# Performance work log

Hardware: AMD Instinct MI355X
Metric: run time of the kernel (lower is better)

Reference implementation:

```python
import jax, jax.numpy as jnp
import numpy as np

B, H, E, V = 128, 1024, 1024, 40000
L, S, A = 256, 10, 10
L_S, L_A = 1.0, 1.0  # s_copy_lambda / a_copy_lambda
NEG = -1e24


def setup_inputs():
    key = jax.random.key(0)
    ks = jax.random.split(key, 32)
    n = lambda i, shape: jax.random.normal(ks[i], shape, dtype=jnp.float32)
    p = lambda i, shape: jax.random.normal(ks[i], shape, dtype=jnp.float32) * 0.02
    rnn_in = 3 * E + H  # embed + history ctx (H) + state ctx (E) + action ctx (E)
    return {
        "inp": n(0, (B, 1, E)),
        "hidden": n(1, (1, B, H)),
        "hs_vectors": n(2, (B, L, H)),
        "state_gumbel_prob": jax.random.uniform(ks[3], (B, S, V), dtype=jnp.float32),
        "state_gumbel_embed": n(4, (B, S, E)),
        "action_gumbel_prob": jax.random.uniform(ks[5], (B, A, V), dtype=jnp.float32),
        "action_gumbel_embed": n(6, (B, A, E)),
        "history_lens": jax.random.randint(ks[7], (B,), 1, L + 1),
        "history_word_indices": jax.random.randint(ks[8], (B, L), 0, V),
        # history word mlp-attention
        "Wq_hist": p(9, (H, H)), "bq_hist": jnp.zeros((H,), jnp.float32),
        "Wm_hist": p(10, (H, H)), "v_hist": p(11, (H,)),
        # init_s_attn / init_a_attn (query H, memory E)
        "Wq_s": p(12, (H, H)), "bq_s": jnp.zeros((H,), jnp.float32),
        "Wm_s": p(13, (E, H)), "v_s": p(14, (H,)),
        "Wq_a": p(15, (H, H)), "bq_a": jnp.zeros((H,), jnp.float32),
        "Wm_a": p(16, (E, H)), "v_a": p(17, (H,)),
        # sparse_copy_attn (memory E+1)
        "Wq_sc": p(18, (H, H)), "bq_sc": jnp.zeros((H,), jnp.float32),
        "Wm_sc": p(19, (E + 1, H)), "v_sc": p(20, (H,)),
        # GRU (torch layout: [3H, in], gate order r,z,n)
        "W_ih": p(21, (3 * H, rnn_in)), "W_hh": p(22, (3 * H, H)),
        "b_ih": jnp.zeros((3 * H,), jnp.float32), "b_hh": jnp.zeros((3 * H,), jnp.float32),
        # output projection
        "W_out": p(23, (H, V)), "b_out": jnp.zeros((V,), jnp.float32),
    }


def _mlp_scores(q, mem, Wq, bq, Wm, v):
    # q: [B,1,H], mem: [B,L,M] -> additive-attention logits [B,1,L]
    t = jnp.tanh((q @ Wq + bq) + (mem @ Wm))  # [B,L,H]
    return (t @ v)[:, None, :]


def reference(inp, hidden, hs_vectors, state_gumbel_prob, state_gumbel_embed,
              action_gumbel_prob, action_gumbel_embed, history_lens,
              history_word_indices, Wq_hist, bq_hist, Wm_hist, v_hist,
              Wq_s, bq_s, Wm_s, v_s, Wq_a, bq_a, Wm_a, v_a,
              Wq_sc, bq_sc, Wm_sc, v_sc, W_ih, W_hh, b_ih, b_hh, W_out, b_out):
    q0 = jnp.transpose(hidden, (1, 0, 2))  # [B,1,H]
    # --- history word attention (masked mlp attention) ---
    hist_scores = _mlp_scores(q0, hs_vectors, Wq_hist, bq_hist, Wm_hist, v_hist)
    valid = jnp.arange(L)[None, None, :] < history_lens[:, None, None]
    hist_scores = jnp.where(valid, hist_scores, NEG)
    c_his = jax.nn.softmax(hist_scores, axis=-1) @ hs_vectors  # [B,1,H]
    # --- init_consult over state / action gumbel embeddings ---
    sw = jax.nn.softmax(_mlp_scores(q0, state_gumbel_embed, Wq_s, bq_s, Wm_s, v_s), axis=-1)
    c_state = sw @ state_gumbel_embed  # [B,1,E]
    aw = jax.nn.softmax(_mlp_scores(q0, action_gumbel_embed, Wq_a, bq_a, Wm_a, v_a), axis=-1)
    c_action = aw @ action_gumbel_embed  # [B,1,E]
    x = jnp.concatenate([inp, c_his, c_state, c_action], axis=-1)[:, 0, :]  # [B,3E+H]
    # --- single-step GRU cell (torch semantics, gate order r,z,n) ---
    h0 = hidden[0]
    gi = x @ W_ih.T + b_ih
    gh = h0 @ W_hh.T + b_hh
    ir, iz, inn = jnp.split(gi, 3, axis=-1)
    hr, hz, hn = jnp.split(gh, 3, axis=-1)
    r = jax.nn.sigmoid(ir + hr)
    z = jax.nn.sigmoid(iz + hz)
    nact = jnp.tanh(inn + r * hn)
    h_new = (1.0 - z) * nact + z * h0  # [B,H]
    # --- vocab logits + copy logits, joint softmax ---
    gene_logits = h_new @ W_out + b_out  # [B,V]
    cq = h_new[:, None, :]
    hs_logits = jnp.einsum('bqh,blh->bql', cq, hs_vectors)[:, 0, :]  # dot attn, [B,L]
    s_tag = jnp.zeros((B, S, 1), jnp.float32)
    a_tag = jnp.ones((B, A, 1), jnp.float32)
    st_logits = _mlp_scores(cq, jnp.concatenate([state_gumbel_embed, s_tag], -1), Wq_sc, bq_sc, Wm_sc, v_sc)[:, 0, :]
    ac_logits = _mlp_scores(cq, jnp.concatenate([action_gumbel_embed, a_tag], -1), Wq_sc, bq_sc, Wm_sc, v_sc)[:, 0, :]
    all_logits = jnp.concatenate([gene_logits, hs_logits, st_logits, ac_logits], axis=-1)
    wp = jax.nn.softmax(all_logits, axis=-1)  # [B, V+L+S+A]
    gene_p = wp[:, :V]
    hs_w = wp[:, V:V + L]
    st_w = wp[:, V + L:V + L + S]
    ac_w = wp[:, V + L + S:]
    # --- copy-distribution mixing ---
    scp = jnp.einsum('bs,bsv->bv', st_w, state_gumbel_prob)
    acp = jnp.einsum('ba,bav->bv', ac_w, action_gumbel_prob)
    gene_p = gene_p + L_S * scp + L_A * acp
    copy_p = jnp.zeros((B, V), jnp.float32).at[jnp.arange(B)[:, None], history_word_indices].add(hs_w)
    out = jnp.log(gene_p + copy_p)[:, None, :]  # [B,1,V]
    return out, h_new[None]
```

## Files before the change

kernel.cpp:

```cpp
#include <hip/hip_runtime.h>
#include <stdint.h>

typedef __attribute__((ext_vector_type(4))) float f32x4;
typedef __attribute__((ext_vector_type(2))) unsigned int u32x2;
typedef __attribute__((ext_vector_type(4))) unsigned int u32x4;
typedef __attribute__((ext_vector_type(8))) short bf16x8;

#define BV (128*40000)

__device__ __forceinline__ unsigned rne_bf16(float f) {
    unsigned x = __float_as_uint(f);
    return ((x + 0x7FFFu + ((x >> 16) & 1u)) >> 16) & 0xFFFFu;
}
__device__ __forceinline__ unsigned pack2(float a, float b) {
    return rne_bf16(a) | (rne_bf16(b) << 16);
}
__device__ __forceinline__ float bf2f(unsigned u) {
    return __uint_as_float((u & 0xFFFFu) << 16);
}
__device__ __forceinline__ float sigm(float x) { return 1.0f / (1.0f + expf(-x)); }

__device__ __forceinline__ void gload16(const void* g, void* l) {
    __builtin_amdgcn_global_load_lds(
        (const __attribute__((address_space(1))) unsigned*)g,
        (__attribute__((address_space(3))) unsigned*)l, 16, 0, 0);
}

template<int EPI>
__device__ __forceinline__ void mgemm(
    const unsigned short* __restrict__ A, const unsigned short* __restrict__ Bt,
    float* __restrict__ out, const float* __restrict__ rb,
    const float* __restrict__ cb1, const float* __restrict__ cb2,
    const float* __restrict__ vvec,
    int m0, int n0, int kb, int ke, int ldk, int ldc, int rpb)
{
    __shared__ unsigned short As[2][4096];
    __shared__ unsigned short Bs[2][4096];
    const int t = threadIdx.x, lane = t & 63, wv = t >> 6;
    const int l16 = lane & 15, lq = lane >> 4;
    const int wm = wv >> 1, wn = wv & 1;

    const int srow = lane >> 2, scol = (lane & 3) << 3;
    const unsigned short* gA0 = A + (size_t)(m0 + (wv << 4) + srow) * ldk + kb + scol;
    const unsigned short* gA1 = gA0 + (size_t)64 * ldk;
    const unsigned short* gB0 = Bt + (size_t)(n0 + (wv << 4) + srow) * ldk + kb + scol;
    const unsigned short* gB1 = gB0 + (size_t)64 * ldk;
    unsigned short* lA0 = &As[0][wv << 9];
    unsigned short* lA1 = &As[0][(wv + 4) << 9];
    unsigned short* lB0 = &Bs[0][wv << 9];
    unsigned short* lB1 = &Bs[0][(wv + 4) << 9];

    f32x4 acc[4][4];
#pragma unroll
    for (int i = 0; i < 4; ++i)
#pragma unroll
        for (int j = 0; j < 4; ++j) acc[i][j] = (f32x4){0.f, 0.f, 0.f, 0.f};

    const int NS = (ke - kb) >> 5;
    gload16(gA0, lA0); gload16(gA1, lA1);
    gload16(gB0, lB0); gload16(gB1, lB1);

    for (int s = 0; s < NS; ++s) {
        __syncthreads();
        if (s + 1 < NS) {
            const int nb = (s + 1) & 1, ko = (s + 1) << 5;
            gload16(gA0 + ko, lA0 + (nb << 12)); gload16(gA1 + ko, lA1 + (nb << 12));
            gload16(gB0 + ko, lB0 + (nb << 12)); gload16(gB1 + ko, lB1 + (nb << 12));
        }
        const unsigned short* ab = As[s & 1];
        const unsigned short* bb = Bs[s & 1];
        bf16x8 af[4], bfv[4];
#pragma unroll
        for (int i = 0; i < 4; ++i)
            af[i] = *(const bf16x8*)(ab + (((wm << 6) + (i << 4) + l16) << 5) + (lq << 3));
#pragma unroll
        for (int i = 0; i < 4; ++i)
            bfv[i] = *(const bf16x8*)(bb + (((wn << 6) + (i << 4) + l16) << 5) + (lq << 3));
#pragma unroll
        for (int mf = 0; mf < 4; ++mf)
#pragma unroll
            for (int nf = 0; nf < 4; ++nf)
                acc[mf][nf] = __builtin_amdgcn_mfma_f32_16x16x32_bf16(af[mf], bfv[nf], acc[mf][nf], 0, 0, 0);
    }

    if (EPI == 1) {
#pragma unroll
        for (int mf = 0; mf < 4; ++mf) {
#pragma unroll
            for (int r = 0; r < 4; ++r) {
                int gr = m0 + (wm << 6) + (mf << 4) + (lq << 2) + r;
                const float* rbp = rb + (size_t)(gr / rpb) * 1024;
                float s = 0.0f;
#pragma unroll
                for (int nf = 0; nf < 4; ++nf) {
                    int gc = n0 + (wn << 6) + (nf << 4) + l16;
                    float xv = acc[mf][nf][r] + rbp[gc] + cb1[gc];
                    if (cb2) xv += cb2[gc];
                    s += tanhf(xv) * vvec[gc];
                }
#pragma unroll
                for (int msk = 1; msk < 16; msk <<= 1) s += __shfl_xor(s, msk, 64);
                if (l16 == 0) atomicAdd(&out[gr], s);
            }
        }
    } else {
#pragma unroll
        for (int mf = 0; mf < 4; ++mf) {
            int gr0 = m0 + (wm << 6) + (mf << 4) + (lq << 2);
#pragma unroll
            for (int nf = 0; nf < 4; ++nf) {
                int gc = n0 + (wn << 6) + (nf << 4) + l16;
#pragma unroll
                for (int r = 0; r < 4; ++r)
                    atomicAdd(&out[(size_t)(gr0 + r) * ldc + gc], acc[mf][nf][r]);
            }
        }
    }
}

__device__ __forceinline__ void gene_body(
    const unsigned short* __restrict__ hnb, const float* __restrict__ Wout,
    const float* __restrict__ b_out, float* __restrict__ out, int n0)
{
    __shared__ unsigned short As[2][4096];
    __shared__ unsigned short Bs[2][4096];
    const int t = threadIdx.x, lane = t & 63, wv = t >> 6;
    const int l16 = lane & 15, lq = lane >> 4;
    const int wm = wv >> 1, wn = wv & 1;

    const int srow = lane >> 2, scol = (lane & 3) << 3;
    const unsigned short* gA0 = hnb + (size_t)((wv << 4) + srow) * 1024 + scol;
    const unsigned short* gA1 = gA0 + (size_t)64 * 1024;
    unsigned short* lA0 = &As[0][wv << 9];
    unsigned short* lA1 = &As[0][(wv + 4) << 9];

    const int bn = t & 127, kh = t >> 7;
    const bool ok = (n0 + bn) < 40000;
    const float* gB = Wout + (size_t)(kh * 16) * 40000 + (n0 + bn);

    f32x4 acc[4][4];
#pragma unroll
    for (int i = 0; i < 4; ++i)
#pragma unroll
        for (int j = 0; j < 4; ++j) acc[i][j] = (f32x4){0.f, 0.f, 0.f, 0.f};

    auto stageB = [&](int buf, int ko) {
        const float* src = gB + (size_t)ko * 40000;
        float f[16];
#pragma unroll
        for (int j = 0; j < 16; ++j) f[j] = ok ? src[(size_t)j * 40000] : 0.0f;
        u32x4* d = (u32x4*)&Bs[buf][bn * 32 + kh * 16];
        d[0] = (u32x4){pack2(f[0],f[1]), pack2(f[2],f[3]), pack2(f[4],f[5]), pack2(f[6],f[7])};
        d[1] = (u32x4){pack2(f[8],f[9]), pack2(f[10],f[11]), pack2(f[12],f[13]), pack2(f[14],f[15])};
    };

    gload16(gA0, lA0); gload16(gA1, lA1); stageB(0, 0);
    for (int s = 0; s < 32; ++s) {
        __syncthreads();
        if (s + 1 < 32) {
            const int nb = (s + 1) & 1, ko = (s + 1) << 5;
            gload16(gA0 + ko, lA0 + (nb << 12)); gload16(gA1 + ko, lA1 + (nb << 12));
            stageB(nb, ko);
        }
        const unsigned short* ab = As[s & 1];
        const unsigned short* bb = Bs[s & 1];
        bf16x8 af[4], bfv[4];
#pragma unroll
        for (int i = 0; i < 4; ++i)
            af[i] = *(const bf16x8*)(ab + (((wm << 6) + (i << 4) + l16) << 5) + (lq << 3));
#pragma unroll
        for (int i = 0; i < 4; ++i)
            bfv[i] = *(const bf16x8*)(bb + (((wn << 6) + (i << 4) + l16) << 5) + (lq << 3));
#pragma unroll
        for (int mf = 0; mf < 4; ++mf)
#pragma unroll
            for (int nf = 0; nf < 4; ++nf)
                acc[mf][nf] = __builtin_amdgcn_mfma_f32_16x16x32_bf16(af[mf], bfv[nf], acc[mf][nf], 0, 0, 0);
    }
#pragma unroll
    for (int mf = 0; mf < 4; ++mf) {
        int gr0 = (wm << 6) + (mf << 4) + (lq << 2);
#pragma unroll
        for (int nf = 0; nf < 4; ++nf) {
            int gc = n0 + (wn << 6) + (nf << 4) + l16;
            if (gc < 40000) {
                float bo = b_out[gc];
#pragma unroll
                for (int r = 0; r < 4; ++r)
                    out[(size_t)(gr0 + r) * 40000 + gc] = acc[mf][nf][r] + bo;
            }
        }
    }
}

__global__ __launch_bounds__(256) void k_hist_att(
    const unsigned short* hs, const unsigned short* WmhT, const int* lens,
    const float* qh_h, const float* bq_h, const float* v_h, float* hsc,
    const unsigned short* se, const unsigned short* ae,
    const unsigned short* WmsT, const unsigned short* WmaT,
    const float* qh_s, const float* qh_a, const float* bq_s, const float* bq_a,
    const float* v_s, const float* v_a, float* stsc, float* acsc) {
    int id = blockIdx.x;
    if (id < 2048) {
        int p = id & 255, n = id >> 8;
        int b = p >> 1, l0 = (p & 1) << 7;
        if (lens[b] <= l0) return;
        mgemm<1>(hs, WmhT, hsc, qh_h, bq_h, nullptr, v_h, p << 7, n << 7, 0, 1024, 1024, 0, 256);
    } else {
        int r = id - 2048;
        int z = r / 80; r -= z * 80;
        int y = r >> 3, x = r & 7;
        if (z == 0)
            mgemm<1>(se, WmsT, stsc, qh_s, bq_s, nullptr, v_s, y * 128, x * 128, 0, 1024, 1024, 0, 10);
        else
            mgemm<1>(ae, WmaT, acsc, qh_a, bq_a, nullptr, v_a, y * 128, x * 128, 0, 1024, 1024, 0, 10);
    }
}

__global__ __launch_bounds__(256) void k_stac3(
    const unsigned short* se, const unsigned short* ae, const unsigned short* WmscT,
    const float* tagrow, const float* qsc, const float* bq_sc, const float* v_sc,
    float* stlg, float* aclg) {
    if (blockIdx.z == 0)
        mgemm<1>(se, WmscT, stlg, qsc, bq_sc, nullptr, v_sc, blockIdx.y * 128, blockIdx.x * 128, 0, 1024, 1024, 0, 10);
    else
        mgemm<1>(ae, WmscT, aclg, qsc, bq_sc, tagrow, v_sc, blockIdx.y * 128, blockIdx.x * 128, 0, 1024, 1024, 0, 10);
}

__global__ __launch_bounds__(256) void k_qh4(
    const unsigned short* q0, const unsigned short* W0, const unsigned short* W1,
    const unsigned short* W2, float* o0, float* o1, float* o2) {
    const unsigned short* W = W0; float* o = o0;
    if (blockIdx.z == 1) { W = W1; o = o1; }
    if (blockIdx.z == 2) { W = W2; o = o2; }
    int kb = blockIdx.y << 8;
    mgemm<2>(q0, W, o, nullptr, nullptr, nullptr, nullptr, 0, blockIdx.x * 128, kb, kb + 256, 1024, 1024, 1);
}

__global__ __launch_bounds__(256) void k_gigh2(
    const unsigned short* xb, const unsigned short* q0,
    const unsigned short* Wih, const unsigned short* Whh, float* gi, float* gh) {
    if (blockIdx.z == 0) {
        int kb = blockIdx.y << 9;
        mgemm<2>(xb, Wih, gi, nullptr, nullptr, nullptr, nullptr, 0, blockIdx.x * 128, kb, kb + 512, 4096, 3072, 1);
    } else {
        if (blockIdx.y >= 2) return;
        int kb = blockIdx.y << 9;
        mgemm<2>(q0, Whh, gh, nullptr, nullptr, nullptr, nullptr, 0, blockIdx.x * 128, kb, kb + 512, 1024, 3072, 1);
    }
}

__global__ __launch_bounds__(256) void k_qsc_gene(
    const unsigned short* hnb, const unsigned short* WqscT, float* qsc,
    const float* Wout, const float* b_out, float* out) {
    int id = blockIdx.x;
    if (id < 16) {
        int x = id & 7, kb = (id >> 3) << 9;
        mgemm<2>(hnb, WqscT, qsc, nullptr, nullptr, nullptr, nullptr, 0, x * 128, kb, kb + 512, 1024, 1024, 1);
    } else {
        gene_body(hnb, Wout, b_out, out, (id - 16) << 7);
    }
}

struct CvtArgs { const float* s[6]; unsigned short* d[6]; int pre[7]; };
__global__ __launch_bounds__(256) void k_cvt_all(CvtArgs a) {
    int total = a.pre[6];
    for (int i = blockIdx.x * 256 + threadIdx.x; i < total; i += gridDim.x * 256) {
        int seg = 0;
        while (i >= a.pre[seg + 1]) ++seg;
        int loc = i - a.pre[seg];
        const f32x4* s4 = (const f32x4*)a.s[seg] + (size_t)loc * 2;
        f32x4 q0 = s4[0], q1 = s4[1];
        ((u32x4*)a.d[seg])[loc] =
            (u32x4){pack2(q0[0],q0[1]), pack2(q0[2],q0[3]), pack2(q1[0],q1[1]), pack2(q1[2],q1[3])};
    }
}

struct TrArgs { const float* s[8]; unsigned short* d[8]; };
__global__ __launch_bounds__(256) void k_trcvt(TrArgs a) {
    __shared__ float tile[64][65];
    const float* in = a.s[blockIdx.z];
    unsigned short* ot = a.d[blockIdx.z];
    int k0 = blockIdx.y << 6, n0 = blockIdx.x << 6;
    int tr = threadIdx.x >> 6, tc = threadIdx.x & 63;
#pragma unroll
    for (int i = 0; i < 16; ++i) {
        int r = (i << 2) + tr;
        tile[r][tc] = in[(size_t)(k0 + r) * 1024 + n0 + tc];
    }
    __syncthreads();
#pragma unroll
    for (int i = 0; i < 16; ++i) {
        int r = (i << 2) + tr;
        ot[(size_t)(n0 + r) * 1024 + k0 + tc] = (unsigned short)rne_bf16(tile[tc][r]);
    }
}

__device__ __forceinline__ void softmax10(const float* src, float* dst) {
    float m = src[0];
    for (int i = 1; i < 10; ++i) m = fmaxf(m, src[i]);
    float z = 0.f, e[10];
    for (int i = 0; i < 10; ++i) { e[i] = expf(src[i] - m); z += e[i]; }
    float iz = 1.0f / z;
    for (int i = 0; i < 10; ++i) dst[i] = e[i] * iz;
}

__global__ __launch_bounds__(256) void k_ctx(
    const float* __restrict__ scores, const int* __restrict__ lens,
    const unsigned short* __restrict__ hs,
    const float* __restrict__ inp, const float* __restrict__ st_sc, const float* __restrict__ ac_sc,
    const unsigned short* __restrict__ se, const unsigned short* __restrict__ ae,
    unsigned short* __restrict__ xb) {
    int b = blockIdx.x, t = threadIdx.x;
    __shared__ float w[256];
    __shared__ float red[256];
    __shared__ float sw[10], aw[10];
    int len = lens[b];
    float s = scores[b * 256 + t];
    bool valid = t < len;
    red[t] = valid ? s : -3.0e38f;
    __syncthreads();
    for (int st = 128; st > 0; st >>= 1) { if (t < st) red[t] = fmaxf(red[t], red[t + st]); __syncthreads(); }
    float m = red[0];
    __syncthreads();
    float e = valid ? expf(s - m) : 0.0f;
    red[t] = e;
    __syncthreads();
    for (int st = 128; st > 0; st >>= 1) { if (t < st) red[t] += red[t + st]; __syncthreads(); }
    float Z = red[0];
    __syncthreads();
    w[t] = e / Z;
    if (t == 0) softmax10(st_sc + b * 10, sw);
    if (t == 64) softmax10(ac_sc + b * 10, aw);
    f32x4 iv = ((const f32x4*)(inp + (size_t)b * 1024))[t];
    *((u32x2*)(xb + (size_t)b * 4096) + t) = (u32x2){pack2(iv[0], iv[1]), pack2(iv[2], iv[3])};
    __syncthreads();
    float a0 = 0.f, a1 = 0.f, a2 = 0.f, a3 = 0.f;
    for (int l = 0; l < 256; ++l) {
        float wl = w[l];
        if (wl == 0.0f) continue;
        u32x2 u = *((const u32x2*)(hs + ((size_t)b * 256 + l) * 1024) + t);
        a0 += wl * bf2f(u[0]); a1 += wl * bf2f(u[0] >> 16);
        a2 += wl * bf2f(u[1]); a3 += wl * bf2f(u[1] >> 16);
    }
    *((u32x2*)(xb + (size_t)b * 4096 + 1024) + t) = (u32x2){pack2(a0, a1), pack2(a2, a3)};
    float cs0=0,cs1=0,cs2=0,cs3=0, ca0=0,ca1=0,ca2=0,ca3=0;
#pragma unroll
    for (int q = 0; q < 10; ++q) {
        u32x2 us = *((const u32x2*)(se + ((size_t)b * 10 + q) * 1024) + t);
        u32x2 ua = *((const u32x2*)(ae + ((size_t)b * 10 + q) * 1024) + t);
        float ws = sw[q], wa = aw[q];
        cs0 += ws * bf2f(us[0]); cs1 += ws * bf2f(us[0] >> 16);
        cs2 += ws * bf2f(us[1]); cs3 += ws * bf2f(us[1] >> 16);
        ca0 += wa * bf2f(ua[0]); ca1 += wa * bf2f(ua[0] >> 16);
        ca2 += wa * bf2f(ua[1]); ca3 += wa * bf2f(ua[1] >> 16);
    }
    *((u32x2*)(xb + (size_t)b * 4096 + 2048) + t) = (u32x2){pack2(cs0, cs1), pack2(cs2, cs3)};
    *((u32x2*)(xb + (size_t)b * 4096 + 3072) + t) = (u32x2){pack2(ca0, ca1), pack2(ca2, ca3)};
}

__global__ __launch_bounds__(1024) void k_gruhsl(
    const float* __restrict__ gi, const float* __restrict__ gh,
    const float* __restrict__ b_ih, const float* __restrict__ b_hh,
    const float* __restrict__ h0, float* __restrict__ hnew,
    unsigned short* __restrict__ hnb,
    const unsigned short* __restrict__ hs, float* __restrict__ hsl) {
    int b = blockIdx.x, j = threadIdx.x;
    size_t i = (size_t)b * 1024 + j;
    const float* gib = gi + (size_t)b * 3072;
    const float* ghb = gh + (size_t)b * 3072;
    float r = sigm(gib[j] + b_ih[j] + ghb[j] + b_hh[j]);
    float z = sigm(gib[1024 + j] + b_ih[1024 + j] + ghb[1024 + j] + b_hh[1024 + j]);
    float hn = ghb[2048 + j] + b_hh[2048 + j];
    float n = tanhf(gib[2048 + j] + b_ih[2048 + j] + r * hn);
    float h = (1.0f - z) * n + z * h0[i];
    hnew[i] = h;
    hnb[i] = (unsigned short)rne_bf16(h);
    __shared__ float hsm[1024];
    hsm[j] = h;
    __syncthreads();
    int wave = j >> 6, lane = j & 63;
    float hr[16];
#pragma unroll
    for (int k = 0; k < 16; ++k) hr[k] = hsm[lane * 16 + k];
    for (int l = wave; l < 256; l += 16) {
        const u32x4* row = (const u32x4*)(hs + ((size_t)b * 256 + l) * 1024);
        u32x4 u0 = row[lane * 2], u1 = row[lane * 2 + 1];
        float s = hr[0]*bf2f(u0[0]) + hr[1]*bf2f(u0[0]>>16) + hr[2]*bf2f(u0[1]) + hr[3]*bf2f(u0[1]>>16)
                + hr[4]*bf2f(u0[2]) + hr[5]*bf2f(u0[2]>>16) + hr[6]*bf2f(u0[3]) + hr[7]*bf2f(u0[3]>>16)
                + hr[8]*bf2f(u1[0]) + hr[9]*bf2f(u1[0]>>16) + hr[10]*bf2f(u1[1]) + hr[11]*bf2f(u1[1]>>16)
                + hr[12]*bf2f(u1[2]) + hr[13]*bf2f(u1[2]>>16) + hr[14]*bf2f(u1[3]) + hr[15]*bf2f(u1[3]>>16);
#pragma unroll
        for (int msk = 1; msk < 64; msk <<= 1) s += __shfl_xor(s, msk, 64);
        if (lane == 0) hsl[b * 256 + l] = s;
    }
}

__global__ __launch_bounds__(256) void k_smsc(
    const float* __restrict__ gene, const float* __restrict__ hsl,
    const float* __restrict__ stl, const float* __restrict__ acl,
    const int* __restrict__ hwi,
    float* __restrict__ mbuf, float* __restrict__ zbuf, float* __restrict__ copyp) {
    int b = blockIdx.x, t = threadIdx.x;
    __shared__ float red[256];
    const f32x4* g4 = (const f32x4*)(gene + (size_t)b * 40000);
    float mx = -3.0e38f;
    for (int i = t; i < 10000; i += 256) {
        f32x4 q = g4[i];
        mx = fmaxf(mx, fmaxf(fmaxf(q[0], q[1]), fmaxf(q[2], q[3])));
    }
    float hv = hsl[b * 256 + t];
    mx = fmaxf(mx, hv);
    if (t < 10) mx = fmaxf(mx, fmaxf(stl[b * 10 + t], acl[b * 10 + t]));
    red[t] = mx; __syncthreads();
    for (int s = 128; s > 0; s >>= 1) { if (t < s) red[t] = fmaxf(red[t], red[t + s]); __syncthreads(); }
    float m = red[0];
    __syncthreads();
    float sum = 0.f;
    for (int i = t; i < 10000; i += 256) {
        f32x4 q = g4[i];
        sum += expf(q[0]-m) + expf(q[1]-m) + expf(q[2]-m) + expf(q[3]-m);
    }
    sum += expf(hv - m);
    if (t < 10) sum += expf(stl[b * 10 + t] - m) + expf(acl[b * 10 + t] - m);
    red[t] = sum; __syncthreads();
    for (int s = 128; s > 0; s >>= 1) { if (t < s) red[t] += red[t + s]; __syncthreads(); }
    float Z = red[0];
    if (t == 0) { mbuf[b] = m; zbuf[b] = Z; }
    float wv = expf(hv - m) / Z;
    atomicAdd(copyp + (size_t)b * 40000 + hwi[b * 256 + t], wv);
}

__global__ __launch_bounds__(256) void k_final(
    float* __restrict__ gene_out, const float* __restrict__ copyp,
    const float* __restrict__ sprob, const float* __restrict__ aprob,
    const float* __restrict__ stl, const float* __restrict__ acl,
    const float* __restrict__ mbuf, const float* __restrict__ zbuf) {
    int b = blockIdx.y, t = threadIdx.x;
    __shared__ float sw[10], aw[10];
    float m = mbuf[b], iz = 1.0f / zbuf[b];
    if (t < 10) sw[t] = expf(stl[b * 10 + t] - m) * iz;
    if (t >= 64 && t < 74) aw[t - 64] = expf(acl[b * 10 + (t - 64)] - m) * iz;
    __syncthreads();
    int v4 = blockIdx.x * 256 + t;
    if (v4 < 10000) {
        size_t base = (size_t)b * 10000 + v4;
        f32x4 g = ((const f32x4*)gene_out)[base];
        f32x4 c = ((const f32x4*)copyp)[base];
        f32x4 acc;
#pragma unroll
        for (int j = 0; j < 4; ++j) acc[j] = expf(g[j] - m) * iz + c[j];
#pragma unroll
        for (int s = 0; s < 10; ++s) {
            f32x4 pv = ((const f32x4*)sprob)[((size_t)b * 10 + s) * 10000 + v4];
            f32x4 av = ((const f32x4*)aprob)[((size_t)b * 10 + s) * 10000 + v4];
            float ws = sw[s], wa = aw[s];
#pragma unroll
            for (int j = 0; j < 4; ++j) acc[j] += ws * pv[j] + wa * av[j];
        }
        f32x4 r;
#pragma unroll
        for (int j = 0; j < 4; ++j) r[j] = logf(acc[j]);
        ((f32x4*)gene_out)[base] = r;
    }
}

#define OFF_QH_H  0
#define OFF_QH_S  131072
#define OFF_QH_A  262144
#define OFF_QSC   393216
#define OFF_GI    524288
#define OFF_GH    917504
#define OFF_HSC   1310720
#define OFF_STSC  1343488
#define OFF_ACSC  1344768
#define OFF_STLG  1346048
#define OFF_ACLG  1347328
#define ZERO_FLOATS 1348608
#define OFF_HSL   1348608
#define OFF_M     1381376
#define OFF_Z     1381504
#define OFF_COPY  1381632
#define FLOAT_TOTAL 6501632
#define SO_HS     0
#define SO_SE     33554432
#define SO_AE     34865152
#define SO_Q0     36175872
#define SO_X      36306944
#define SO_HNB    36831232
#define SO_WQHT   36962304
#define SO_WQST   38010880
#define SO_WQAT   39059456
#define SO_WQSCT  40108032
#define SO_WMHT   41156608
#define SO_WMST   42205184
#define SO_WMAT   43253760
#define SO_WMSCT  44302336
#define SO_WIH    45350912
#define SO_WHH    57933824

extern "C" void kernel_launch(void* const* d_in, const int* in_sizes, int n_in,
                              void* d_out, int out_size, void* d_ws, size_t ws_size,
                              hipStream_t stream) {
    const float* inp     = (const float*)d_in[0];
    const float* hidden  = (const float*)d_in[1];
    const float* hs      = (const float*)d_in[2];
    const float* sprob   = (const float*)d_in[3];
    const float* se      = (const float*)d_in[4];
    const float* aprob   = (const float*)d_in[5];
    const float* ae      = (const float*)d_in[6];
    const int*   lens    = (const int*)d_in[7];
    const int*   hwi     = (const int*)d_in[8];
    const float* Wq_hist = (const float*)d_in[9];
    const float* bq_hist = (const float*)d_in[10];
    const float* Wm_hist = (const float*)d_in[11];
    const float* v_hist  = (const float*)d_in[12];
    const float* Wq_s    = (const float*)d_in[13];
    const float* bq_s    = (const float*)d_in[14];
    const float* Wm_s    = (const float*)d_in[15];
    const float* v_s     = (const float*)d_in[16];
    const float* Wq_a    = (const float*)d_in[17];
    const float* bq_a    = (const float*)d_in[18];
    const float* Wm_a    = (const float*)d_in[19];
    const float* v_a     = (const float*)d_in[20];
    const float* Wq_sc   = (const float*)d_in[21];
    const float* bq_sc   = (const float*)d_in[22];
    const float* Wm_sc   = (const float*)d_in[23];
    const float* v_sc    = (const float*)d_in[24];
    const float* W_ih    = (const float*)d_in[25];
    const float* W_hh    = (const float*)d_in[26];
    const float* b_ih    = (const float*)d_in[27];
    const float* b_hh    = (const float*)d_in[28];
    const float* W_out   = (const float*)d_in[29];
    const float* b_out   = (const float*)d_in[30];

    float* out  = (float*)d_out;
    float* w    = (float*)d_ws;
    float* hnew = out + BV;
    unsigned short* sb = (unsigned short*)(w + FLOAT_TOTAL);

    float* qh_h = w + OFF_QH_H;  float* qh_s = w + OFF_QH_S;  float* qh_a = w + OFF_QH_A;
    float* qsc  = w + OFF_QSC;   float* gi   = w + OFF_GI;    float* gh   = w + OFF_GH;
    float* hsc  = w + OFF_HSC;   float* stsc = w + OFF_STSC;  float* acsc = w + OFF_ACSC;
    float* stlg = w + OFF_STLG;  float* aclg = w + OFF_ACLG;
    float* hsl  = w + OFF_HSL;   float* mbuf = w + OFF_M;     float* zbuf = w + OFF_Z;
    float* copyp = w + OFF_COPY;

    unsigned short* hs_bf = sb + SO_HS;   unsigned short* se_bf = sb + SO_SE;
    unsigned short* ae_bf = sb + SO_AE;   unsigned short* q0_bf = sb + SO_Q0;
    unsigned short* x_bf  = sb + SO_X;    unsigned short* hnb   = sb + SO_HNB;
    unsigned short* WqhT  = sb + SO_WQHT; unsigned short* WqsT  = sb + SO_WQST;
    unsigned short* WqaT  = sb + SO_WQAT; unsigned short* WqscT = sb + SO_WQSCT;
    unsigned short* WmhT  = sb + SO_WMHT; unsigned short* WmsT  = sb + SO_WMST;
    unsigned short* WmaT  = sb + SO_WMAT; unsigned short* WmscT = sb + SO_WMSCT;
    unsigned short* WihB  = sb + SO_WIH;  unsigned short* WhhB  = sb + SO_WHH;

    dim3 blk(256);

    hipMemsetAsync(w, 0, (size_t)ZERO_FLOATS * 4, stream);
    hipMemsetAsync(copyp, 0, (size_t)BV * 4, stream);

    CvtArgs ca;
    ca.s[0]=hs; ca.s[1]=se; ca.s[2]=ae; ca.s[3]=hidden; ca.s[4]=W_ih; ca.s[5]=W_hh;
    ca.d[0]=hs_bf; ca.d[1]=se_bf; ca.d[2]=ae_bf; ca.d[3]=q0_bf; ca.d[4]=WihB; ca.d[5]=WhhB;
    ca.pre[0]=0; ca.pre[1]=4194304; ca.pre[2]=4358144; ca.pre[3]=4521984;
    ca.pre[4]=4538368; ca.pre[5]=6111232; ca.pre[6]=6504448;
    k_cvt_all<<<dim3(4096), blk, 0, stream>>>(ca);

    TrArgs ta;
    ta.s[0]=Wq_hist; ta.s[1]=Wq_s; ta.s[2]=Wq_a; ta.s[3]=Wq_sc;
    ta.s[4]=Wm_hist; ta.s[5]=Wm_s; ta.s[6]=Wm_a; ta.s[7]=Wm_sc;
    ta.d[0]=WqhT; ta.d[1]=WqsT; ta.d[2]=WqaT; ta.d[3]=WqscT;
    ta.d[4]=WmhT; ta.d[5]=WmsT; ta.d[6]=WmaT; ta.d[7]=WmscT;
    k_trcvt<<<dim3(16, 16, 8), blk, 0, stream>>>(ta);

    k_qh4<<<dim3(8, 4, 3), blk, 0, stream>>>(q0_bf, WqhT, WqsT, WqaT, qh_h, qh_s, qh_a);
    k_hist_att<<<dim3(2208), blk, 0, stream>>>(hs_bf, WmhT, lens, qh_h, bq_hist, v_hist, hsc,
                                               se_bf, ae_bf, WmsT, WmaT, qh_s, qh_a, bq_s, bq_a,
                                               v_s, v_a, stsc, acsc);
    k_ctx<<<dim3(128), blk, 0, stream>>>(hsc, lens, hs_bf, inp, stsc, acsc, se_bf, ae_bf, x_bf);
    k_gigh2<<<dim3(24, 8, 2), blk, 0, stream>>>(x_bf, q0_bf, WihB, WhhB, gi, gh);
    k_gruhsl<<<dim3(128), dim3(1024), 0, stream>>>(gi, gh, b_ih, b_hh, hidden, hnew, hnb, hs_bf, hsl);
    k_qsc_gene<<<dim3(329), blk, 0, stream>>>(hnb, WqscT, qsc, W_out, b_out, out);
    k_stac3<<<dim3(8, 10, 2), blk, 0, stream>>>(se_bf, ae_bf, WmscT, Wm_sc + (size_t)1024 * 1024,
                                                qsc, bq_sc, v_sc, stlg, aclg);
    k_smsc<<<dim3(128), blk, 0, stream>>>(out, hsl, stlg, aclg, hwi, mbuf, zbuf, copyp);
    k_final<<<dim3(40, 128), blk, 0, stream>>>(out, copyp, sprob, aprob, stlg, aclg, mbuf, zbuf);

    (void)in_sizes; (void)n_in; (void)out_size; (void)ws_size;
}
```

Measured before the change: 591.2 us.

## Replace history/state/action attention GEMM with 256x256-tile 512-thread kernel

Replaces the 128x128-tile attention-scoring kernel with a new kernel using 256x256 tiles, 512 threads, 64-wide K steps and XOR-swizzled LDS, giving more data reuse per block. Work is skipped at 16-row granularity using per-batch history lengths, and a bijective block-id remap spreads tiles across XCDs. It also swaps tanhf for a fast exp-based tanh in all MLP-attention epilogues. The large tile with one block per CU lowers occupancy and makes length-based skipping coarser at the block level, and the fast tanh changes numerics slightly.

```diff
diff --git a/kernel.cpp b/kernel.cpp
--- a/kernel.cpp
+++ b/kernel.cpp
@@ -19,11 +19,152 @@
     return __uint_as_float((u & 0xFFFFu) << 16);
 }
 __device__ __forceinline__ float sigm(float x) { return 1.0f / (1.0f + expf(-x)); }
+__device__ __forceinline__ float ftanh(float x) {
+    float e = __expf(2.0f * x);
+    return 1.0f - 2.0f / (e + 1.0f);
+}
 
 __device__ __forceinline__ void gload16(const void* g, void* l) {
     __builtin_amdgcn_global_load_lds(
         (const __attribute__((address_space(1))) unsigned*)g,
         (__attribute__((address_space(3))) unsigned*)l, 16, 0, 0);
+}
+
+struct BigArgs {
+    const unsigned short *hs, *WmhT, *se, *ae, *WmsT, *WmaT;
+    const int* lens;
+    const float *qh_h, *bq_h, *v_h;
+    const float *qh_s, *bq_s, *v_s;
+    const float *qh_a, *bq_a, *v_a;
+    float *hsc, *stsc, *acsc;
+};
+
+__global__ __launch_bounds__(512, 1) void k_big(BigArgs a) {
+    __shared__ unsigned short As[2][16384];
+    __shared__ unsigned short Bs[2][16384];
+
+    int bid = blockIdx.x;
+    int wg = (bid & 7) * 69 + (bid >> 3);
+
+    const unsigned short *A, *Bt;
+    const float *rb, *cb, *vv;
+    float* out;
+    int m0, n0, vrows, rpb;
+    if (wg < 512) {
+        int m = wg >> 2, n = wg & 3;
+        A = a.hs; Bt = a.WmhT; rb = a.qh_h; cb = a.bq_h; vv = a.v_h; out = a.hsc;
+        m0 = m << 8; n0 = n << 8; vrows = a.lens[m]; rpb = 256;
+    } else {
+        int r = wg - 512;
+        int op = r / 20; r -= op * 20;
+        int mt = r >> 2, nt = r & 3;
+        if (op == 0) { A = a.se; Bt = a.WmsT; rb = a.qh_s; cb = a.bq_s; vv = a.v_s; out = a.stsc; }
+        else         { A = a.ae; Bt = a.WmaT; rb = a.qh_a; cb = a.bq_a; vv = a.v_a; out = a.acsc; }
+        m0 = mt << 8; n0 = nt << 8; vrows = 256; rpb = 10;
+    }
+
+    const int t = threadIdx.x, lane = t & 63, wv = t >> 6;
+    const int l16 = lane & 15, lq = lane >> 4;
+    const int wm = wv >> 2, wn = wv & 3;
+
+    const int srowL = t >> 3;
+    const int gccA = ((t & 7) ^ (srowL & 7)) << 3;
+    const unsigned short* gA = A + (size_t)(m0 + srowL) * 1024 + gccA;
+    const unsigned short* gB = Bt + (size_t)(n0 + srowL) * 1024 + gccA;
+
+    f32x4 acc[8][4];
+#pragma unroll
+    for (int i = 0; i < 8; ++i)
+#pragma unroll
+        for (int j = 0; j < 4; ++j) acc[i][j] = (f32x4){0.f, 0.f, 0.f, 0.f};
+
+    const int sw = l16 & 7;
+    const int c0 = ((lq ^ sw) << 3);
+    const int A0 = (wm << 13) + (l16 << 6);
+    const int B0 = ((wn >> 1) << 13) + ((((wn & 1) << 6) + l16) << 6);
+
+#define STAGE(kt, d)                                                          \
+    {                                                                         \
+        const unsigned short* ga_ = gA + (size_t)(kt) * 64;                   \
+        const unsigned short* gb_ = gB + (size_t)(kt) * 64;                   \
+        _Pragma("unroll")                                                     \
+        for (int h_ = 0; h_ < 2; ++h_) {                                      \
+            _Pragma("unroll")                                                 \
+            for (int r_ = 0; r_ < 2; ++r_) {                                  \
+                size_t go_ = (size_t)(h_ * 128 + r_ * 64) * 1024;             \
+                int lo_ = h_ * 8192 + r_ * 4096 + (wv << 9);                  \
+                gload16(ga_ + go_, &As[d][lo_]);                              \
+                gload16(gb_ + go_, &Bs[d][lo_]);                              \
+            }                                                                 \
+        }                                                                     \
+    }
+
+    STAGE(0, 0);
+    for (int kt = 0; kt < 16; ++kt) {
+        int cur = kt & 1;
+        if (kt < 15) {
+            STAGE(kt + 1, cur ^ 1);
+            asm volatile("s_waitcnt vmcnt(8)" ::: "memory");
+        } else {
+            asm volatile("s_waitcnt vmcnt(0)" ::: "memory");
+        }
+        __builtin_amdgcn_s_barrier();
+        __builtin_amdgcn_sched_barrier(0);
+
+        const unsigned short* ab = As[cur];
+        const unsigned short* bb = Bs[cur];
+        if (vrows > (wm << 7)) {
+            bf16x8 bf[4][2];
+#pragma unroll
+            for (int nf = 0; nf < 4; ++nf) {
+                bf[nf][0] = *(const bf16x8*)(bb + B0 + (nf << 10) + c0);
+                bf[nf][1] = *(const bf16x8*)(bb + B0 + (nf << 10) + (c0 ^ 32));
+            }
+#pragma unroll
+            for (int mf = 0; mf < 8; ++mf) {
+                if ((wm << 7) + (mf << 4) < vrows) {
+                    bf16x8 a0 = *(const bf16x8*)(ab + A0 + (mf << 10) + c0);
+                    bf16x8 a1 = *(const bf16x8*)(ab + A0 + (mf << 10) + (c0 ^ 32));
+#pragma unroll
+                    for (int nf = 0; nf < 4; ++nf) {
+                        acc[mf][nf] = __builtin_amdgcn_mfma_f32_16x16x32_bf16(a0, bf[nf][0], acc[mf][nf], 0, 0, 0);
+                        acc[mf][nf] = __builtin_amdgcn_mfma_f32_16x16x32_bf16(a1, bf[nf][1], acc[mf][nf], 0, 0, 0);
+                    }
+                }
+            }
+        }
+        __builtin_amdgcn_sched_barrier(0);
+        __builtin_amdgcn_s_barrier();
+    }
+#undef STAGE
+
+    float cbv[4], vvv[4];
+    int gcs[4];
+#pragma unroll
+    for (int nf = 0; nf < 4; ++nf) {
+        int gc = n0 + (wn << 6) + (nf << 4) + l16;
+        gcs[nf] = gc; cbv[nf] = cb[gc]; vvv[nf] = vv[gc];
+    }
+#pragma unroll
+    for (int mf = 0; mf < 8; ++mf) {
+        int rloc = (wm << 7) + (mf << 4);
+        if (rloc < vrows) {
+#pragma unroll
+            for (int r = 0; r < 4; ++r) {
+                int gr = m0 + rloc + (lq << 2) + r;
+                const float* rbp = rb + (size_t)(gr / rpb) * 1024;
+                float s = 0.f;
+#pragma unroll
+                for (int nf = 0; nf < 4; ++nf) {
+                    float x = acc[mf][nf][r] + rbp[gcs[nf]] + cbv[nf];
+                    s += ftanh(x) * vvv[nf];
+                }
+#pragma unroll
+                for (int m2 = 1; m2 < 16; m2 <<= 1) s += __shfl_xor(s, m2, 64);
+                if (l16 == 0) atomicAdd(&out[gr], s);
+            }
+        }
+    }
 }
 
 template<int EPI>
@@ -96,7 +237,7 @@
                     int gc = n0 + (wn << 6) + (nf << 4) + l16;
                     float xv = acc[mf][nf][r] + rbp[gc] + cb1[gc];
                     if (cb2) xv += cb2[gc];
-                    s += tanhf(xv) * vvec[gc];
+                    s += ftanh(xv) * vvec[gc];
                 }
 #pragma unroll
                 for (int msk = 1; msk < 16; msk <<= 1) s += __shfl_xor(s, msk, 64);
@@ -190,30 +331,6 @@
                     out[(size_t)(gr0 + r) * 40000 + gc] = acc[mf][nf][r] + bo;
             }
         }
-    }
-}
-
-__global__ __launch_bounds__(256) void k_hist_att(
-    const unsigned short* hs, const unsigned short* WmhT, const int* lens,
-    const float* qh_h, const float* bq_h, const float* v_h, float* hsc,
-    const unsigned short* se, const unsigned short* ae,
-    const unsigned short* WmsT, const unsigned short* WmaT,
-    const float* qh_s, const float* qh_a, const float* bq_s, const float* bq_a,
-    const float* v_s, const float* v_a, float* stsc, float* acsc) {
-    int id = blockIdx.x;
-    if (id < 2048) {
-        int p = id & 255, n = id >> 8;
-        int b = p >> 1, l0 = (p & 1) << 7;
-        if (lens[b] <= l0) return;
-        mgemm<1>(hs, WmhT, hsc, qh_h, bq_h, nullptr, v_h, p << 7, n << 7, 0, 1024, 1024, 0, 256);
-    } else {
-        int r = id - 2048;
-        int z = r / 80; r -= z * 80;
-        int y = r >> 3, x = r & 7;
-        if (z == 0)
-            mgemm<1>(se, WmsT, stsc, qh_s, bq_s, nullptr, v_s, y * 128, x * 128, 0, 1024, 1024, 0, 10);
-        else
-            mgemm<1>(ae, WmaT, acsc, qh_a, bq_a, nullptr, v_a, y * 128, x * 128, 0, 1024, 1024, 0, 10);
     }
 }
 
@@ -575,9 +692,16 @@
     k_trcvt<<<dim3(16, 16, 8), blk, 0, stream>>>(ta);
 
     k_qh4<<<dim3(8, 4, 3), blk, 0, stream>>>(q0_bf, WqhT, WqsT, WqaT, qh_h, qh_s, qh_a);
-    k_hist_att<<<dim3(2208), blk, 0, stream>>>(hs_bf, WmhT, lens, qh_h, bq_hist, v_hist, hsc,
-                                               se_bf, ae_bf, WmsT, WmaT, qh_s, qh_a, bq_s, bq_a,
-                                               v_s, v_a, stsc, acsc);
+
+    BigArgs ba;
+    ba.hs = hs_bf; ba.WmhT = WmhT; ba.se = se_bf; ba.ae = ae_bf;
+    ba.WmsT = WmsT; ba.WmaT = WmaT; ba.lens = lens;
+    ba.qh_h = qh_h; ba.bq_h = bq_hist; ba.v_h = v_hist;
+    ba.qh_s = qh_s; ba.bq_s = bq_s; ba.v_s = v_s;
+    ba.qh_a = qh_a; ba.bq_a = bq_a; ba.v_a = v_a;
+    ba.hsc = hsc; ba.stsc = stsc; ba.acsc = acsc;
+    k_big<<<dim3(552), dim3(512), 0, stream>>>(ba);
+
     k_ctx<<<dim3(128), blk, 0, stream>>>(hsc, lens, hs_bf, inp, stsc, acsc, se_bf, ae_bf, x_bf);
     k_gigh2<<<dim3(24, 8, 2), blk, 0, stream>>>(x_bf, q0_bf, WihB, WhhB, gi, gh);
     k_gruhsl<<<dim3(128), dim3(1024), 0, stream>>>(gi, gh, b_ih, b_hh, hidden, hnew, hnb, hs_bf, hsl);
```

Measured after the change: 575.4 us. -2.7%, faster.
